# Optimization experiments

Measured on AMD Instinct MI355X. Metric: run time of the kernel, lower is better.

## Reference

```python
import jax, jax.numpy as jnp
import numpy as np

B, E, H, T = 32768, 64, 128, 12  # batch, embedding_dim, decoder_h_dim, pred_len


def setup_inputs() -> dict:
    key = jax.random.key(0)
    ks = jax.random.split(key, 13)
    f = lambda k, shape: jax.random.normal(k, shape, dtype=jnp.float32) * 0.05
    return {
        "last_pos": f(ks[0], (B, 2)),
        "last_pos_rel": f(ks[1], (B, 2)),
        "h0": f(ks[2], (1, B, H)),
        "c0": f(ks[3], (1, B, H)),
        "pred_ped_speed": jax.random.uniform(ks[4], (T, B, 1), dtype=jnp.float32),
        # spatial_embedding: Linear(3, E)
        "W_se": f(ks[5], (E, 3)),
        "b_se": f(ks[6], (E,)),
        # single-layer LSTM(E -> H), torch gate order [i, f, g, o]
        "W_ih": f(ks[7], (4 * H, E)),
        "W_hh": f(ks[8], (4 * H, H)),
        "b_ih": f(ks[9], (4 * H,)),
        "b_hh": f(ks[10], (4 * H,)),
        # hidden2pos: Linear(H, 2)
        "W_hp": f(ks[11], (2, H)),
        "b_hp": f(ks[12], (2,)),
    }


def reference(last_pos, last_pos_rel, h0, c0, pred_ped_speed,
              W_se, b_se, W_ih, W_hh, b_ih, b_hh, W_hp, b_hp):
    # train_or_test == 0 path: speed comes straight from pred_ped_speed
    Tlen = pred_ped_speed.shape[0]
    b_lstm = b_ih + b_hh
    # initial decoder input: embed concat([last_pos_rel, speed_0])  -> [B, E]
    x0 = jnp.concatenate([last_pos_rel, pred_ped_speed[0]], axis=1) @ W_se.T + b_se

    def step(carry, t):
        h, c, x, lp = carry  # h,c: [B,H]; x: [B,E]; lp: [B,2]
        gates = x @ W_ih.T + h @ W_hh.T + b_lstm           # [B, 4H]
        i, f_, g, o = jnp.split(gates, 4, axis=1)
        c = jax.nn.sigmoid(f_) * c + jax.nn.sigmoid(i) * jnp.tanh(g)
        h = jax.nn.sigmoid(o) * jnp.tanh(c)
        rel = h @ W_hp.T + b_hp                            # [B, 2]
        lp = rel + lp                                      # curr_pos -> last_pos
        # speed for next step; at final step torch keeps the previous speed
        spd = pred_ped_speed[jnp.minimum(t + 1, Tlen - 1)]
        x = jnp.concatenate([rel, spd], axis=1) @ W_se.T + b_se
        return (h, c, x, lp), rel

    (h, c, _, _), rels = jax.lax.scan(
        step, (h0[0], c0[0], x0, last_pos), jnp.arange(Tlen))
    # pred_traj_fake_rel: [T, B, 2]; final hidden state: [1, B, H]
    return rels, h[None]
```

## Files before the change

kernel.cpp:

```cpp
#include <hip/hip_runtime.h>

#define T_LEN 12
#define B_N   32768
#define H_N   128
#define BM    64

typedef __attribute__((ext_vector_type(8))) __bf16 bf16x8;
typedef __attribute__((ext_vector_type(8))) short  short8v;
typedef __attribute__((ext_vector_type(4))) float  f32x4;

__device__ __forceinline__ unsigned short f2bf(float f) {
  unsigned int u = __builtin_bit_cast(unsigned int, f);
  u += 0x7fffu + ((u >> 16) & 1u);
  return (unsigned short)(u >> 16);
}
__device__ __forceinline__ float sigm(float x) {
  return __builtin_amdgcn_rcpf(1.f + __builtin_amdgcn_exp2f(-1.4426950408889634f * x));
}
__device__ __forceinline__ float tanh_(float x) {
  return 1.f - 2.f * __builtin_amdgcn_rcpf(__builtin_amdgcn_exp2f(2.8853900817779268f * x) + 1.f);
}

__global__ void prep_kernel(const float* __restrict__ Wih, const float* __restrict__ Whh,
                            const float* __restrict__ bih, const float* __restrict__ bhh,
                            const float* __restrict__ Wse, const float* __restrict__ bse,
                            const float* __restrict__ Whp, const float* __restrict__ bhp,
                            unsigned short* __restrict__ WfReg, unsigned short* __restrict__ WfGO,
                            unsigned short* __restrict__ pBg, float* __restrict__ u,
                            float* __restrict__ w0, float* __restrict__ G) {
  int i = blockIdx.x * 256 + threadIdx.x;
  if (i < 65536) {
    int row = i >> 7, k = i & 127;
    float s = Whh[row * 128 + k];
    float wh0 = Whp[k], wh1 = Whp[128 + k];
    for (int e = 0; e < 64; ++e)
      s += Wih[row * 64 + e] * (Wse[e * 3 + 0] * wh0 + Wse[e * 3 + 1] * wh1);
    unsigned short v = f2bf(s);
    int g = row >> 7, unit = row & 127, w = unit >> 4, l15 = unit & 15;
    int ks = k >> 5, kg = (k >> 3) & 3, j = k & 7, l = kg * 16 + l15;
    if (g < 2) WfReg[((g * 4 + ks) * 512 + w * 64 + l) * 8 + j] = v;
    else       WfGO[(((g - 2) * 4 + ks) * 512 + w * 64 + l) * 8 + j] = v;
  } else if (i < 65536 + 2048) {
    int j = i - 65536;
    int n = j >> 2, which = j & 3;
    float s = 0.f;
    if (which < 2) {
      for (int e = 0; e < 64; ++e) s += Wih[n * 64 + e] * Wse[e * 3 + which];
      G[n * 2 + which] = s;
    } else if (which == 2) {
      for (int e = 0; e < 64; ++e) s += Wih[n * 64 + e] * Wse[e * 3 + 2];
      u[n] = s;
    } else {
      for (int e = 0; e < 64; ++e)
        s += Wih[n * 64 + e] * (bse[e] + Wse[e * 3 + 0] * bhp[0] + Wse[e * 3 + 1] * bhp[1]);
      w0[n] = bih[n] + bhh[n] + s;
    }
  } else if (i < 65536 + 2048 + 2048) {
    int idx = i - 65536 - 2048;
    int ks = idx >> 9, l = (idx >> 3) & 63, j = idx & 7;
    int c = l & 15, kg = l >> 4;
    pBg[idx] = (c < 2) ? f2bf(Whp[c * 128 + ks * 32 + kg * 8 + j]) : (unsigned short)0;
  }
}

__launch_bounds__(1024, 4)
__global__ void decoder_kernel(const float* __restrict__ lpr,
                               const float* __restrict__ h0,
                               const float* __restrict__ c0,
                               const float* __restrict__ pps,
                               const float* __restrict__ Whp,
                               const float* __restrict__ bhp,
                               const unsigned short* __restrict__ WfReg,
                               const unsigned short* __restrict__ WfGO,
                               const unsigned short* __restrict__ pBg,
                               const float* __restrict__ u,
                               const float* __restrict__ w0,
                               const float* __restrict__ G,
                               float* __restrict__ out_rel,
                               float* __restrict__ out_h) {
  __shared__ unsigned short WgoL[32768];
  __shared__ unsigned short hA[2][BM * 128];
  __shared__ unsigned short pBL[2048];
  __shared__ float spdL[T_LEN * BM];
  __shared__ float dbuf[BM * 2];
  __shared__ float GL[1024];

  const int tid  = threadIdx.x;
  const int wav  = tid >> 6;
  const int wc   = wav & 7;
  const int wr   = wav >> 3;
  const int l    = tid & 63;
  const int l15  = l & 15;
  const int lg   = l >> 4;
  const int brow = blockIdx.x * BM;
  const int nh   = wc * 16 + l15;
  const int rowb = wr * 32;
  const int swzA = (l15 & 7) << 4;

  short8v bw[2][4];
#pragma unroll
  for (int g = 0; g < 2; ++g)
#pragma unroll
    for (int ks = 0; ks < 4; ++ks)
      bw[g][ks] = *(const short8v*)(WfReg + ((g * 4 + ks) * 512 + wc * 64 + l) * 8);
#pragma unroll
  for (int it = 0; it < 4; ++it) {
    int idx = it * 1024 + tid;
    *(short8v*)(WgoL + idx * 8) = *(const short8v*)(WfGO + idx * 8);
  }
  if (tid < 256) *(short8v*)(pBL + tid * 8) = *(const short8v*)(pBg + tid * 8);
  GL[tid & 1023] = G[tid & 1023];
  if (tid < T_LEN * BM) spdL[tid] = pps[(tid >> 6) * B_N + brow + (tid & 63)];

  float w0r[4], ur[4];
#pragma unroll
  for (int g = 0; g < 4; ++g) { w0r[g] = w0[g * 128 + nh]; ur[g] = u[g * 128 + nh]; }

  f32x4 cst[2];
#pragma unroll
  for (int rt = 0; rt < 2; ++rt)
#pragma unroll
    for (int r = 0; r < 4; ++r)
      cst[rt][r] = c0[(brow + rowb + rt * 16 + lg * 4 + r) * H_N + nh];

  {
    int row = tid >> 4, k0 = (tid & 15) * 8;
    const float* src = h0 + (brow + row) * H_N + k0;
    unsigned short tmp[8];
#pragma unroll
    for (int j = 0; j < 8; ++j) tmp[j] = f2bf(src[j]);
    *(short8v*)((char*)&hA[0][0] + ((row * 256 + k0 * 2) ^ ((row & 7) << 4))) = *(short8v*)tmp;
  }
  {
    int dot = tid >> 3, part = tid & 7;
    int row = dot >> 1, jj = dot & 1;
    float s = 0.f;
    const float* hrow = h0 + (brow + row) * H_N + part * 16;
    const float* wrow = Whp + jj * 128 + part * 16;
#pragma unroll
    for (int k = 0; k < 16; ++k) s += hrow[k] * wrow[k];
    s += __shfl_xor(s, 1); s += __shfl_xor(s, 2); s += __shfl_xor(s, 4);
    if (part == 0) dbuf[dot] = lpr[(brow + row) * 2 + jj] - bhp[jj] - s;
  }
  const float bhpr = (l15 < 2) ? bhp[l15] : 0.f;

  char* rb = (char*)&hA[0][0];
  char* wbuf = (char*)&hA[1][0];

#pragma unroll 1
  for (int t = 0; t < T_LEN; ++t) {
    __syncthreads();
    f32x4 relC = (f32x4){0.f, 0.f, 0.f, 0.f};

#pragma unroll
    for (int rt = 0; rt < 2; ++rt) {
      f32x4 acc[4];
#pragma unroll
      for (int g = 0; g < 4; ++g) acc[g] = (f32x4){w0r[g], w0r[g], w0r[g], w0r[g]};

#pragma unroll
      for (int ks = 0; ks < 4; ++ks) {
        bf16x8 a = __builtin_bit_cast(bf16x8,
            *(short8v*)(rb + (((rowb + rt * 16 + l15) * 256 + ks * 64 + lg * 16) ^ swzA)));
        bf16x8 bg = __builtin_bit_cast(bf16x8, *(short8v*)(WgoL + (ks * 512 + wc * 64 + l) * 8));
        bf16x8 bo = __builtin_bit_cast(bf16x8, *(short8v*)(WgoL + ((4 + ks) * 512 + wc * 64 + l) * 8));
        acc[0] = __builtin_amdgcn_mfma_f32_16x16x32_bf16(a, __builtin_bit_cast(bf16x8, bw[0][ks]), acc[0], 0, 0, 0);
        acc[1] = __builtin_amdgcn_mfma_f32_16x16x32_bf16(a, __builtin_bit_cast(bf16x8, bw[1][ks]), acc[1], 0, 0, 0);
        acc[2] = __builtin_amdgcn_mfma_f32_16x16x32_bf16(a, bg, acc[2], 0, 0, 0);
        acc[3] = __builtin_amdgcn_mfma_f32_16x16x32_bf16(a, bo, acc[3], 0, 0, 0);
        if (wc == rt && t > 0) {
          bf16x8 pb = __builtin_bit_cast(bf16x8, *(short8v*)(pBL + (ks * 64 + l) * 8));
          relC = __builtin_amdgcn_mfma_f32_16x16x32_bf16(a, pb, relC, 0, 0, 0);
        }
      }
      if (t == 0) {
#pragma unroll
        for (int r = 0; r < 4; ++r) {
          int row = rowb + rt * 16 + lg * 4 + r;
          float d0 = dbuf[row * 2 + 0], d1 = dbuf[row * 2 + 1];
#pragma unroll
          for (int g = 0; g < 4; ++g)
            acc[g][r] += d0 * GL[(g * 128 + nh) * 2 + 0] + d1 * GL[(g * 128 + nh) * 2 + 1];
        }
      }
#pragma unroll
      for (int r = 0; r < 4; ++r) {
        int row = rowb + rt * 16 + lg * 4 + r;
        float spd = spdL[t * BM + row];
        float gi = __builtin_fmaf(spd, ur[0], acc[0][r]);
        float gf = __builtin_fmaf(spd, ur[1], acc[1][r]);
        float gg = __builtin_fmaf(spd, ur[2], acc[2][r]);
        float go = __builtin_fmaf(spd, ur[3], acc[3][r]);
        float cn = sigm(gf) * cst[rt][r] + sigm(gi) * tanh_(gg);
        cst[rt][r] = cn;
        float h = sigm(go) * tanh_(cn);
        *(unsigned short*)(wbuf + ((row * 256 + nh * 2) ^ ((row & 7) << 4))) = f2bf(h);
        if (t == T_LEN - 1) out_h[(brow + row) * H_N + nh] = h;
      }
    }
    if (wc < 2 && t > 0 && l15 < 2) {
#pragma unroll
      for (int r = 0; r < 4; ++r)
        out_rel[(size_t)(t - 1) * B_N * 2 + (brow + rowb + wc * 16 + lg * 4 + r) * 2 + l15] = relC[r] + bhpr;
    }
    char* tmpp = rb; rb = wbuf; wbuf = tmpp;
  }

  __syncthreads();
  if (wc < 2) {
    f32x4 relC = (f32x4){0.f, 0.f, 0.f, 0.f};
#pragma unroll
    for (int ks = 0; ks < 4; ++ks) {
      bf16x8 a = __builtin_bit_cast(bf16x8,
          *(short8v*)(rb + (((rowb + wc * 16 + l15) * 256 + ks * 64 + lg * 16) ^ swzA)));
      bf16x8 pb = __builtin_bit_cast(bf16x8, *(short8v*)(pBL + (ks * 64 + l) * 8));
      relC = __builtin_amdgcn_mfma_f32_16x16x32_bf16(a, pb, relC, 0, 0, 0);
    }
    if (l15 < 2) {
#pragma unroll
      for (int r = 0; r < 4; ++r)
        out_rel[(size_t)(T_LEN - 1) * B_N * 2 + (brow + rowb + wc * 16 + lg * 4 + r) * 2 + l15] = relC[r] + bhpr;
    }
  }
}

extern "C" void kernel_launch(void* const* d_in, const int* in_sizes, int n_in,
                              void* d_out, int out_size, void* d_ws, size_t ws_size,
                              hipStream_t stream) {
  const float* lpr  = (const float*)d_in[1];
  const float* h0   = (const float*)d_in[2];
  const float* c0   = (const float*)d_in[3];
  const float* pps  = (const float*)d_in[4];
  const float* W_se = (const float*)d_in[5];
  const float* b_se = (const float*)d_in[6];
  const float* W_ih = (const float*)d_in[7];
  const float* W_hh = (const float*)d_in[8];
  const float* b_ih = (const float*)d_in[9];
  const float* b_hh = (const float*)d_in[10];
  const float* W_hp = (const float*)d_in[11];
  const float* b_hp = (const float*)d_in[12];

  unsigned short* WfReg = (unsigned short*)d_ws;
  unsigned short* WfGO  = (unsigned short*)((char*)d_ws + 65536);
  unsigned short* pBg   = (unsigned short*)((char*)d_ws + 131072);
  float* u  = (float*)((char*)d_ws + 135168);
  float* w0 = (float*)((char*)d_ws + 137216);
  float* G  = (float*)((char*)d_ws + 139264);

  float* out_rel = (float*)d_out;
  float* out_h   = out_rel + (size_t)T_LEN * B_N * 2;

  hipLaunchKernelGGL(prep_kernel, dim3((65536 + 4096 + 255) / 256), dim3(256), 0, stream,
                     W_ih, W_hh, b_ih, b_hh, W_se, b_se, W_hp, b_hp,
                     WfReg, WfGO, pBg, u, w0, G);
  hipLaunchKernelGGL(decoder_kernel, dim3(B_N / BM), dim3(1024), 0, stream,
                     lpr, h0, c0, pps, W_hp, b_hp, WfReg, WfGO, pBg, u, w0, G,
                     out_rel, out_h);
}
```

Measured before the change: 231.6 us.

## Stage all gate weights in LDS, single h buffer, prescale activations

All four gate weight slices now live in LDS instead of two being held in registers. The hidden-state buffer goes from double to single, with an extra barrier between the MFMA phase and the activation-write phase. The MFMA loop is reordered so each B fragment is reused across both row tiles. The sigmoid/tanh exponent scale factors are folded into the prepped weights and biases, which removes per-element multiplies. The aim is to cut register pressure and ALU work at the cost of more LDS traffic, plus one more barrier per timestep.

```diff
diff --git a/kernel.cpp b/kernel.cpp
--- a/kernel.cpp
+++ b/kernel.cpp
@@ -14,20 +14,25 @@
   u += 0x7fffu + ((u >> 16) & 1u);
   return (unsigned short)(u >> 16);
 }
-__device__ __forceinline__ float sigm(float x) {
-  return __builtin_amdgcn_rcpf(1.f + __builtin_amdgcn_exp2f(-1.4426950408889634f * x));
-}
-__device__ __forceinline__ float tanh_(float x) {
-  return 1.f - 2.f * __builtin_amdgcn_rcpf(__builtin_amdgcn_exp2f(2.8853900817779268f * x) + 1.f);
+__device__ __forceinline__ float sigm_p(float x) {
+  return __builtin_amdgcn_rcpf(1.f + __builtin_amdgcn_exp2f(x));
+}
+__device__ __forceinline__ float tanh_p(float x) {
+  return __builtin_fmaf(-2.f, __builtin_amdgcn_rcpf(__builtin_amdgcn_exp2f(x) + 1.f), 1.f);
+}
+__device__ __forceinline__ float tanh_c(float x) {
+  return tanh_p(2.8853900817779268f * x);
 }
 
 __global__ void prep_kernel(const float* __restrict__ Wih, const float* __restrict__ Whh,
                             const float* __restrict__ bih, const float* __restrict__ bhh,
                             const float* __restrict__ Wse, const float* __restrict__ bse,
                             const float* __restrict__ Whp, const float* __restrict__ bhp,
-                            unsigned short* __restrict__ WfReg, unsigned short* __restrict__ WfGO,
-                            unsigned short* __restrict__ pBg, float* __restrict__ u,
-                            float* __restrict__ w0, float* __restrict__ G) {
+                            unsigned short* __restrict__ WfA, unsigned short* __restrict__ pBg,
+                            float* __restrict__ u, float* __restrict__ w0,
+                            float* __restrict__ G) {
+  const float SCL[4] = {-1.4426950408889634f, -1.4426950408889634f,
+                         2.8853900817779268f, -1.4426950408889634f};
   int i = blockIdx.x * 256 + threadIdx.x;
   if (i < 65536) {
     int row = i >> 7, k = i & 127;
@@ -35,25 +40,23 @@
     float wh0 = Whp[k], wh1 = Whp[128 + k];
     for (int e = 0; e < 64; ++e)
       s += Wih[row * 64 + e] * (Wse[e * 3 + 0] * wh0 + Wse[e * 3 + 1] * wh1);
-    unsigned short v = f2bf(s);
     int g = row >> 7, unit = row & 127, w = unit >> 4, l15 = unit & 15;
     int ks = k >> 5, kg = (k >> 3) & 3, j = k & 7, l = kg * 16 + l15;
-    if (g < 2) WfReg[((g * 4 + ks) * 512 + w * 64 + l) * 8 + j] = v;
-    else       WfGO[(((g - 2) * 4 + ks) * 512 + w * 64 + l) * 8 + j] = v;
+    WfA[((g * 4 + ks) * 512 + w * 64 + l) * 8 + j] = f2bf(s * SCL[g]);
   } else if (i < 65536 + 2048) {
     int j = i - 65536;
-    int n = j >> 2, which = j & 3;
+    int n = j >> 2, which = j & 3, g = n >> 7;
     float s = 0.f;
     if (which < 2) {
       for (int e = 0; e < 64; ++e) s += Wih[n * 64 + e] * Wse[e * 3 + which];
-      G[n * 2 + which] = s;
+      G[n * 2 + which] = s * SCL[g];
     } else if (which == 2) {
       for (int e = 0; e < 64; ++e) s += Wih[n * 64 + e] * Wse[e * 3 + 2];
-      u[n] = s;
+      u[n] = s * SCL[g];
     } else {
       for (int e = 0; e < 64; ++e)
         s += Wih[n * 64 + e] * (bse[e] + Wse[e * 3 + 0] * bhp[0] + Wse[e * 3 + 1] * bhp[1]);
-      w0[n] = bih[n] + bhh[n] + s;
+      w0[n] = (bih[n] + bhh[n] + s) * SCL[g];
     }
   } else if (i < 65536 + 2048 + 2048) {
     int idx = i - 65536 - 2048;
@@ -70,16 +73,15 @@
                                const float* __restrict__ pps,
                                const float* __restrict__ Whp,
                                const float* __restrict__ bhp,
-                               const unsigned short* __restrict__ WfReg,
-                               const unsigned short* __restrict__ WfGO,
+                               const unsigned short* __restrict__ WfA,
                                const unsigned short* __restrict__ pBg,
                                const float* __restrict__ u,
                                const float* __restrict__ w0,
                                const float* __restrict__ G,
                                float* __restrict__ out_rel,
                                float* __restrict__ out_h) {
-  __shared__ unsigned short WgoL[32768];
-  __shared__ unsigned short hA[2][BM * 128];
+  __shared__ unsigned short WfL[65536];
+  __shared__ unsigned short hA[BM * 128];
   __shared__ unsigned short pBL[2048];
   __shared__ float spdL[T_LEN * BM];
   __shared__ float dbuf[BM * 2];
@@ -96,17 +98,12 @@
   const int nh   = wc * 16 + l15;
   const int rowb = wr * 32;
   const int swzA = (l15 & 7) << 4;
-
-  short8v bw[2][4];
-#pragma unroll
-  for (int g = 0; g < 2; ++g)
-#pragma unroll
-    for (int ks = 0; ks < 4; ++ks)
-      bw[g][ks] = *(const short8v*)(WfReg + ((g * 4 + ks) * 512 + wc * 64 + l) * 8);
-#pragma unroll
-  for (int it = 0; it < 4; ++it) {
+  char* hB = (char*)hA;
+
+#pragma unroll
+  for (int it = 0; it < 8; ++it) {
     int idx = it * 1024 + tid;
-    *(short8v*)(WgoL + idx * 8) = *(const short8v*)(WfGO + idx * 8);
+    *(short8v*)(WfL + idx * 8) = *(const short8v*)(WfA + idx * 8);
   }
   if (tid < 256) *(short8v*)(pBL + tid * 8) = *(const short8v*)(pBg + tid * 8);
   GL[tid & 1023] = G[tid & 1023];
@@ -129,7 +126,7 @@
     unsigned short tmp[8];
 #pragma unroll
     for (int j = 0; j < 8; ++j) tmp[j] = f2bf(src[j]);
-    *(short8v*)((char*)&hA[0][0] + ((row * 256 + k0 * 2) ^ ((row & 7) << 4))) = *(short8v*)tmp;
+    *(short8v*)(hB + ((row * 256 + k0 * 2) ^ ((row & 7) << 4))) = *(short8v*)tmp;
   }
   {
     int dot = tid >> 3, part = tid & 7;
@@ -144,35 +141,52 @@
   }
   const float bhpr = (l15 < 2) ? bhp[l15] : 0.f;
 
-  char* rb = (char*)&hA[0][0];
-  char* wbuf = (char*)&hA[1][0];
-
 #pragma unroll 1
   for (int t = 0; t < T_LEN; ++t) {
     __syncthreads();
+
+    f32x4 acc[4][2];
+#pragma unroll
+    for (int g = 0; g < 4; ++g)
+#pragma unroll
+      for (int rt = 0; rt < 2; ++rt)
+        acc[g][rt] = (f32x4){w0r[g], w0r[g], w0r[g], w0r[g]};
     f32x4 relC = (f32x4){0.f, 0.f, 0.f, 0.f};
 
 #pragma unroll
+    for (int ks = 0; ks < 4; ++ks) {
+      bf16x8 a0 = __builtin_bit_cast(bf16x8,
+          *(short8v*)(hB + (((rowb + l15) * 256 + ks * 64 + lg * 16) ^ swzA)));
+      bf16x8 a1 = __builtin_bit_cast(bf16x8,
+          *(short8v*)(hB + (((rowb + 16 + l15) * 256 + ks * 64 + lg * 16) ^ swzA)));
+      bf16x8 b0 = __builtin_bit_cast(bf16x8, *(short8v*)(WfL + ((0 * 4 + ks) * 512 + wc * 64 + l) * 8));
+      bf16x8 b1 = __builtin_bit_cast(bf16x8, *(short8v*)(WfL + ((1 * 4 + ks) * 512 + wc * 64 + l) * 8));
+      bf16x8 b2 = __builtin_bit_cast(bf16x8, *(short8v*)(WfL + ((2 * 4 + ks) * 512 + wc * 64 + l) * 8));
+      bf16x8 b3 = __builtin_bit_cast(bf16x8, *(short8v*)(WfL + ((3 * 4 + ks) * 512 + wc * 64 + l) * 8));
+      acc[0][0] = __builtin_amdgcn_mfma_f32_16x16x32_bf16(a0, b0, acc[0][0], 0, 0, 0);
+      acc[0][1] = __builtin_amdgcn_mfma_f32_16x16x32_bf16(a1, b0, acc[0][1], 0, 0, 0);
+      acc[1][0] = __builtin_amdgcn_mfma_f32_16x16x32_bf16(a0, b1, acc[1][0], 0, 0, 0);
+      acc[1][1] = __builtin_amdgcn_mfma_f32_16x16x32_bf16(a1, b1, acc[1][1], 0, 0, 0);
+      acc[2][0] = __builtin_amdgcn_mfma_f32_16x16x32_bf16(a0, b2, acc[2][0], 0, 0, 0);
+      acc[2][1] = __builtin_amdgcn_mfma_f32_16x16x32_bf16(a1, b2, acc[2][1], 0, 0, 0);
+      acc[3][0] = __builtin_amdgcn_mfma_f32_16x16x32_bf16(a0, b3, acc[3][0], 0, 0, 0);
+      acc[3][1] = __builtin_amdgcn_mfma_f32_16x16x32_bf16(a1, b3, acc[3][1], 0, 0, 0);
+      if (wc < 2 && t > 0) {
+        bf16x8 pb = __builtin_bit_cast(bf16x8, *(short8v*)(pBL + (ks * 64 + l) * 8));
+        relC = __builtin_amdgcn_mfma_f32_16x16x32_bf16(wc == 0 ? a0 : a1, pb, relC, 0, 0, 0);
+      }
+    }
+    if (wc < 2 && t > 0 && l15 < 2) {
+#pragma unroll
+      for (int r = 0; r < 4; ++r)
+        out_rel[(size_t)(t - 1) * B_N * 2 + (brow + rowb + wc * 16 + lg * 4 + r) * 2 + l15] = relC[r] + bhpr;
+    }
+
+    __syncthreads();
+
+#pragma unroll
     for (int rt = 0; rt < 2; ++rt) {
-      f32x4 acc[4];
-#pragma unroll
-      for (int g = 0; g < 4; ++g) acc[g] = (f32x4){w0r[g], w0r[g], w0r[g], w0r[g]};
-
-#pragma unroll
-      for (int ks = 0; ks < 4; ++ks) {
-        bf16x8 a = __builtin_bit_cast(bf16x8,
-            *(short8v*)(rb + (((rowb + rt * 16 + l15) * 256 + ks * 64 + lg * 16) ^ swzA)));
-        bf16x8 bg = __builtin_bit_cast(bf16x8, *(short8v*)(WgoL + (ks * 512 + wc * 64 + l) * 8));
-        bf16x8 bo = __builtin_bit_cast(bf16x8, *(short8v*)(WgoL + ((4 + ks) * 512 + wc * 64 + l) * 8));
-        acc[0] = __builtin_amdgcn_mfma_f32_16x16x32_bf16(a, __builtin_bit_cast(bf16x8, bw[0][ks]), acc[0], 0, 0, 0);
-        acc[1] = __builtin_amdgcn_mfma_f32_16x16x32_bf16(a, __builtin_bit_cast(bf16x8, bw[1][ks]), acc[1], 0, 0, 0);
-        acc[2] = __builtin_amdgcn_mfma_f32_16x16x32_bf16(a, bg, acc[2], 0, 0, 0);
-        acc[3] = __builtin_amdgcn_mfma_f32_16x16x32_bf16(a, bo, acc[3], 0, 0, 0);
-        if (wc == rt && t > 0) {
-          bf16x8 pb = __builtin_bit_cast(bf16x8, *(short8v*)(pBL + (ks * 64 + l) * 8));
-          relC = __builtin_amdgcn_mfma_f32_16x16x32_bf16(a, pb, relC, 0, 0, 0);
-        }
-      }
+      const f32x4 spdv = *(const f32x4*)(spdL + t * BM + rowb + rt * 16 + lg * 4);
       if (t == 0) {
 #pragma unroll
         for (int r = 0; r < 4; ++r) {
@@ -180,30 +194,24 @@
           float d0 = dbuf[row * 2 + 0], d1 = dbuf[row * 2 + 1];
 #pragma unroll
           for (int g = 0; g < 4; ++g)
-            acc[g][r] += d0 * GL[(g * 128 + nh) * 2 + 0] + d1 * GL[(g * 128 + nh) * 2 + 1];
+            acc[g][rt][r] += d0 * GL[(g * 128 + nh) * 2 + 0] + d1 * GL[(g * 128 + nh) * 2 + 1];
         }
       }
 #pragma unroll
       for (int r = 0; r < 4; ++r) {
         int row = rowb + rt * 16 + lg * 4 + r;
-        float spd = spdL[t * BM + row];
-        float gi = __builtin_fmaf(spd, ur[0], acc[0][r]);
-        float gf = __builtin_fmaf(spd, ur[1], acc[1][r]);
-        float gg = __builtin_fmaf(spd, ur[2], acc[2][r]);
-        float go = __builtin_fmaf(spd, ur[3], acc[3][r]);
-        float cn = sigm(gf) * cst[rt][r] + sigm(gi) * tanh_(gg);
+        float spd = spdv[r];
+        float gi = __builtin_fmaf(spd, ur[0], acc[0][rt][r]);
+        float gf = __builtin_fmaf(spd, ur[1], acc[1][rt][r]);
+        float gg = __builtin_fmaf(spd, ur[2], acc[2][rt][r]);
+        float go = __builtin_fmaf(spd, ur[3], acc[3][rt][r]);
+        float cn = sigm_p(gf) * cst[rt][r] + sigm_p(gi) * tanh_p(gg);
         cst[rt][r] = cn;
-        float h = sigm(go) * tanh_(cn);
-        *(unsigned short*)(wbuf + ((row * 256 + nh * 2) ^ ((row & 7) << 4))) = f2bf(h);
+        float h = sigm_p(go) * tanh_c(cn);
+        *(unsigned short*)(hB + ((row * 256 + nh * 2) ^ ((row & 7) << 4))) = f2bf(h);
         if (t == T_LEN - 1) out_h[(brow + row) * H_N + nh] = h;
       }
     }
-    if (wc < 2 && t > 0 && l15 < 2) {
-#pragma unroll
-      for (int r = 0; r < 4; ++r)
-        out_rel[(size_t)(t - 1) * B_N * 2 + (brow + rowb + wc * 16 + lg * 4 + r) * 2 + l15] = relC[r] + bhpr;
-    }
-    char* tmpp = rb; rb = wbuf; wbuf = tmpp;
   }
 
   __syncthreads();
@@ -212,7 +220,7 @@
 #pragma unroll
     for (int ks = 0; ks < 4; ++ks) {
       bf16x8 a = __builtin_bit_cast(bf16x8,
-          *(short8v*)(rb + (((rowb + wc * 16 + l15) * 256 + ks * 64 + lg * 16) ^ swzA)));
+          *(short8v*)(hB + (((rowb + wc * 16 + l15) * 256 + ks * 64 + lg * 16) ^ swzA)));
       bf16x8 pb = __builtin_bit_cast(bf16x8, *(short8v*)(pBL + (ks * 64 + l) * 8));
       relC = __builtin_amdgcn_mfma_f32_16x16x32_bf16(a, pb, relC, 0, 0, 0);
     }
@@ -240,9 +248,8 @@
   const float* W_hp = (const float*)d_in[11];
   const float* b_hp = (const float*)d_in[12];
 
-  unsigned short* WfReg = (unsigned short*)d_ws;
-  unsigned short* WfGO  = (unsigned short*)((char*)d_ws + 65536);
-  unsigned short* pBg   = (unsigned short*)((char*)d_ws + 131072);
+  unsigned short* WfA = (unsigned short*)d_ws;
+  unsigned short* pBg = (unsigned short*)((char*)d_ws + 131072);
   float* u  = (float*)((char*)d_ws + 135168);
   float* w0 = (float*)((char*)d_ws + 137216);
   float* G  = (float*)((char*)d_ws + 139264);
@@ -252,8 +259,8 @@
 
   hipLaunchKernelGGL(prep_kernel, dim3((65536 + 4096 + 255) / 256), dim3(256), 0, stream,
                      W_ih, W_hh, b_ih, b_hh, W_se, b_se, W_hp, b_hp,
-                     WfReg, WfGO, pBg, u, w0, G);
+                     WfA, pBg, u, w0, G);
   hipLaunchKernelGGL(decoder_kernel, dim3(B_N / BM), dim3(1024), 0, stream,
-                     lpr, h0, c0, pps, W_hp, b_hp, WfReg, WfGO, pBg, u, w0, G,
+                     lpr, h0, c0, pps, W_hp, b_hp, WfA, pBg, u, w0, G,
                      out_rel, out_h);
 }
```

Measured after the change: 217.2 us. 1.07x faster.
